# Optimization experiments

Hardware: AMD Instinct MI355X
Metric: run time of the kernel (lower is better)

## Reference

```python
import jax, jax.numpy as jnp
import numpy as np

B, S, D, H = 4, 1024, 1024, 16
HD = D // H  # head_dim = 64


def setup_inputs() -> dict:
    key = jax.random.key(0)
    ks = jax.random.split(key, 12)
    inp = {
        "query": jax.random.normal(ks[0], (B, S, D), jnp.float32),
        "key": jax.random.normal(ks[1], (B, S, D), jnp.float32),
        "value": jax.random.normal(ks[2], (B, S, D), jnp.float32),
        # padding mask: 0 = masked, 1 = keep; broadcastable to [B,H,Sq,Sk]
        "mask": jax.random.randint(ks[3], (B, 1, 1, S), 0, 2, jnp.int32),
        # Dense params (Glorot-ish scale)
        "Wq": jax.random.normal(ks[4], (D, D), jnp.float32) / np.sqrt(D),
        "bq": jnp.zeros((D,), jnp.float32),
        "Wk": jax.random.normal(ks[5], (D, D), jnp.float32) / np.sqrt(D),
        "bk": jnp.zeros((D,), jnp.float32),
        "Wv": jax.random.normal(ks[6], (D, D), jnp.float32) / np.sqrt(D),
        "bv": jnp.zeros((D,), jnp.float32),
        "Wo": jax.random.normal(ks[7], (D, D), jnp.float32) / np.sqrt(D),
        "bo": jnp.zeros((D,), jnp.float32),
    }
    return inp


def _split_heads(x):
    # [B, S, D] -> [B, H, S, HD]
    b, s, _ = x.shape
    return x.reshape(b, s, H, HD).transpose(0, 2, 1, 3)


def reference(query, key, value, mask, Wq, bq, Wk, bk, Wv, bv, Wo, bo):
    q = _split_heads(query @ Wq + bq)   # [B,H,S,HD]
    k = _split_heads(key @ Wk + bk)
    v = _split_heads(value @ Wv + bv)

    scale = jnp.sqrt(jnp.asarray(HD, q.dtype))
    energy = jnp.einsum("bhqd,bhkd->bhqk", q, k) / scale  # [B,H,S,S]
    energy = jnp.where(mask == 0, jnp.asarray(-1e10, energy.dtype), energy)
    attention = jax.nn.softmax(energy, axis=-1)
    # dropout is identity at inference
    x = jnp.einsum("bhqk,bhkd->bhqd", attention, v)       # [B,H,S,HD]
    x = x.transpose(0, 2, 1, 3).reshape(query.shape[0], -1, H * HD)  # [B,S,D]
    outputs = x @ Wo + bo
    return outputs, attention
```

## Files before the change

### kernel.cpp

```cpp
#include <hip/hip_runtime.h>

typedef short short8  __attribute__((ext_vector_type(8)));
typedef short short4v __attribute__((ext_vector_type(4)));
typedef float float4v __attribute__((ext_vector_type(4)));
typedef int   int4v   __attribute__((ext_vector_type(4)));

__device__ __forceinline__ short f2bf(float f) {
    unsigned u = __builtin_bit_cast(unsigned, f);
    u += 0x7fff + ((u >> 16) & 1);
    return (short)(u >> 16);
}

__device__ __forceinline__ void gl_lds16(const void* g, void* l) {
    __builtin_amdgcn_global_load_lds(
        (const __attribute__((address_space(1))) void*)g,
        (__attribute__((address_space(3))) void*)l, 16, 0, 0);
}

__global__ __launch_bounds__(256) void prep(
    const float* __restrict__ W0, const float* __restrict__ W1,
    const float* __restrict__ W2, const float* __restrict__ W3,
    short* __restrict__ T0, short* __restrict__ T1,
    short* __restrict__ T2, short* __restrict__ T3,
    const float* __restrict__ qf, const float* __restrict__ kf,
    const float* __restrict__ vf,
    short* __restrict__ Qb, short* __restrict__ Kb, short* __restrict__ Vb)
{
    __shared__ short Tl[64 * 72];
    const int tid = threadIdx.x;
    if (blockIdx.x >= 1024) {
        int cid = blockIdx.x - 1024;
        int arr = cid >> 11;
        const float* src = arr == 0 ? qf : arr == 1 ? kf : vf;
        short*       dst = arr == 0 ? Qb : arr == 1 ? Kb : Vb;
        size_t base = ((size_t)(cid & 2047) * 256 + tid) * 8;
        float4v v0 = *(const float4v*)&src[base];
        float4v v1 = *(const float4v*)&src[base + 4];
        short8 o = {f2bf(v0[0]), f2bf(v0[1]), f2bf(v0[2]), f2bf(v0[3]),
                    f2bf(v1[0]), f2bf(v1[1]), f2bf(v1[2]), f2bf(v1[3])};
        *(short8*)&dst[base] = o;
        return;
    }
    const int mat = blockIdx.x >> 8;
    const int t   = blockIdx.x & 255;
    const int k0 = (t >> 4) * 64, n0 = (t & 15) * 64;
    const float* W = mat == 0 ? W0 : mat == 1 ? W1 : mat == 2 ? W2 : W3;
    short*       T = mat == 0 ? T0 : mat == 1 ? T1 : mat == 2 ? T2 : T3;
    #pragma unroll
    for (int i = 0; i < 4; i++) {
        int c = tid + i * 256;
        int row = c >> 4, c4 = (c & 15) * 4;
        float4v v = *(const float4v*)&W[(size_t)(k0 + row) * 1024 + n0 + c4];
        short4v s = {f2bf(v[0]), f2bf(v[1]), f2bf(v[2]), f2bf(v[3])};
        *(short4v*)&Tl[row * 72 + c4] = s;
    }
    __syncthreads();
    #pragma unroll
    for (int i = 0; i < 2; i++) {
        int c = tid + i * 256;
        int nrow = c >> 3, k8 = (c & 7) * 8;
        short8 v;
        #pragma unroll
        for (int e = 0; e < 8; e++) v[e] = Tl[(k8 + e) * 72 + nrow];
        *(short8*)&T[(size_t)(n0 + nrow) * 1024 + k0 + k8] = v;
    }
}

__device__ __forceinline__ void gemm_body(
    const short* __restrict__ A, const short* __restrict__ Bt,
    short* As, short* Bs, float4v (&acc)[4][2], int m0, int n0, int K)
{
    const int tid = threadIdx.x;
    const int w = tid >> 6, lid = tid & 63, quad = lid >> 4, l15 = lid & 15;
    const int wr = w >> 1, wc = w & 1;
    const int lrow = lid >> 3, lcb = lid & 7;

    for (int kb = 0; kb < K; kb += 64) {
        #pragma unroll
        for (int p = 0; p < 4; p++) {
            int chunk = p * 4 + w;
            int row = chunk * 8 + lrow;
            int cb = lcb ^ (row & 7);
            gl_lds16(&A[(size_t)(m0 + row) * K + kb + cb * 8], &As[chunk * 512]);
        }
        #pragma unroll
        for (int p = 0; p < 2; p++) {
            int chunk = p * 4 + w;
            int row = chunk * 8 + lrow;
            int cb = lcb ^ (row & 7);
            gl_lds16(&Bt[(size_t)(n0 + row) * K + kb + cb * 8], &Bs[chunk * 512]);
        }
        __syncthreads();

        short8 af[4][2], bfr[2][2];
        #pragma unroll
        for (int i = 0; i < 4; i++) {
            int row = wr * 64 + i * 16 + l15;
            int sw = row & 7;
            #pragma unroll
            for (int h = 0; h < 2; h++)
                af[i][h] = *(short8*)&As[row * 64 + ((h * 4 + quad) ^ sw) * 8];
        }
        #pragma unroll
        for (int j = 0; j < 2; j++) {
            int row = wc * 32 + j * 16 + l15;
            int sw = row & 7;
            #pragma unroll
            for (int h = 0; h < 2; h++)
                bfr[j][h] = *(short8*)&Bs[row * 64 + ((h * 4 + quad) ^ sw) * 8];
        }
        #pragma unroll
        for (int i = 0; i < 4; i++)
            #pragma unroll
            for (int j = 0; j < 2; j++) {
                acc[i][j] = __builtin_amdgcn_mfma_f32_16x16x32_bf16(
                    af[i][0], bfr[j][0], acc[i][j], 0, 0, 0);
                acc[i][j] = __builtin_amdgcn_mfma_f32_16x16x32_bf16(
                    af[i][1], bfr[j][1], acc[i][j], 0, 0, 0);
            }
        __syncthreads();
    }
}

__global__ __launch_bounds__(256) void gemm_qkv(
    const short* __restrict__ Ab, const short* __restrict__ Btb,
    const float* __restrict__ b0, const float* __restrict__ b1,
    const float* __restrict__ b2, short* __restrict__ Cq,
    short* __restrict__ Ck, short* __restrict__ Cvt)
{
    __shared__ short As[128 * 64];
    __shared__ short Bs[64 * 64];
    const int zz = blockIdx.z;
    const short* A  = Ab  + (size_t)zz * 4194304;
    const short* Bt = Btb + (size_t)zz * 1048576;
    const float* bias = zz == 0 ? b0 : zz == 1 ? b1 : b2;
    const int m0 = blockIdx.x * 128, n0 = blockIdx.y * 64;

    float4v acc[4][2];
    #pragma unroll
    for (int i = 0; i < 4; i++)
        #pragma unroll
        for (int j = 0; j < 2; j++) acc[i][j] = (float4v){0.f, 0.f, 0.f, 0.f};

    gemm_body(A, Bt, As, Bs, acc, m0, n0, 1024);

    const int tid = threadIdx.x;
    const int w = tid >> 6, lid = tid & 63, quad = lid >> 4, l15 = lid & 15;
    const int wr = w >> 1, wc = w & 1;
    #pragma unroll
    for (int j = 0; j < 2; j++) {
        int n = n0 + wc * 32 + j * 16 + l15;
        float bj = bias[n];
        #pragma unroll
        for (int i = 0; i < 4; i++) {
            if (zz == 2) {
                int b = m0 >> 10;
                int sbase = (m0 & 1023) + wr * 64 + i * 16 + quad * 4;
                short4v sv;
                #pragma unroll
                for (int r = 0; r < 4; r++) sv[r] = f2bf(acc[i][j][r] + bj);
                *(short4v*)&Cvt[(size_t)b * 1048576 + (size_t)n * 1024 + sbase] = sv;
            } else {
                short* C = zz == 0 ? Cq : Ck;
                #pragma unroll
                for (int r = 0; r < 4; r++) {
                    int m = m0 + wr * 64 + i * 16 + quad * 4 + r;
                    C[(size_t)m * 1024 + n] = f2bf(acc[i][j][r] + bj);
                }
            }
        }
    }
}

__global__ __launch_bounds__(256) void gemm_out(
    const short* __restrict__ A, const short* __restrict__ Bt,
    const float* __restrict__ bias, float* __restrict__ C)
{
    __shared__ short As[128 * 64];
    __shared__ short Bs[64 * 64];
    const int m0 = blockIdx.x * 128, n0 = blockIdx.y * 64;
    float4v acc[4][2];
    #pragma unroll
    for (int i = 0; i < 4; i++)
        #pragma unroll
        for (int j = 0; j < 2; j++) acc[i][j] = (float4v){0.f, 0.f, 0.f, 0.f};

    gemm_body(A, Bt, As, Bs, acc, m0, n0, 1024);

    const int tid = threadIdx.x;
    const int w = tid >> 6, lid = tid & 63, quad = lid >> 4, l15 = lid & 15;
    const int wr = w >> 1, wc = w & 1;
    #pragma unroll
    for (int j = 0; j < 2; j++) {
        int n = n0 + wc * 32 + j * 16 + l15;
        float bj = bias[n];
        #pragma unroll
        for (int i = 0; i < 4; i++)
            #pragma unroll
            for (int r = 0; r < 4; r++) {
                int m = m0 + wr * 64 + i * 16 + quad * 4 + r;
                C[(size_t)m * 1024 + n] = acc[i][j][r] + bj;
            }
    }
}

__global__ __launch_bounds__(256) void attn_kernel(
    const short* __restrict__ Qp, const short* __restrict__ Kp,
    const short* __restrict__ Vt, const int* __restrict__ mask,
    float* __restrict__ attnOut, short* __restrict__ X)
{
    __shared__ float SH[4608];
    __shared__ int   maskl[1024];
    __shared__ float redmx[4][16];
    __shared__ float redsm[4][16];

    const int tid = threadIdx.x;
    const int w = tid >> 6, lid = tid & 63, quad = lid >> 4, l15 = lid & 15;
    const int bid = blockIdx.x;
    const int qb = bid & 63;
    const int bh = bid >> 6;
    const int b = bh >> 4, h = bh & 15;
    const int q0 = qb * 16;
    const size_t rowbase = (size_t)b * 1048576;
    const size_t hoff = (size_t)h * 64;

    *(int4v*)&maskl[tid * 4] = *(const int4v*)&mask[b * 1024 + tid * 4];

    short8 aq0 = *(const short8*)
        &Qp[rowbase + (size_t)(q0 + l15) * 1024 + hoff + quad * 8];
    short8 aq1 = *(const short8*)
        &Qp[rowbase + (size_t)(q0 + l15) * 1024 + hoff + 32 + quad * 8];

    float4v accS[16];
    #pragma unroll
    for (int a = 0; a < 16; a++) accS[a] = (float4v){0.f, 0.f, 0.f, 0.f};

    #pragma unroll
    for (int nk = 0; nk < 8; nk++) {
        #pragma unroll
        for (int jj = 0; jj < 2; jj++) {
            int n = nk * 128 + w * 32 + jj * 16 + l15;
            const short* kr = &Kp[rowbase + (size_t)n * 1024 + hoff + quad * 8];
            short8 b0 = *(const short8*)kr;
            short8 b1 = *(const short8*)(kr + 32);
            int a = nk * 2 + jj;
            accS[a] = __builtin_amdgcn_mfma_f32_16x16x32_bf16(aq0, b0, accS[a], 0, 0, 0);
            accS[a] = __builtin_amdgcn_mfma_f32_16x16x32_bf16(aq1, b1, accS[a], 0, 0, 0);
        }
    }
    __syncthreads();

    float mx[4] = {-3e38f, -3e38f, -3e38f, -3e38f};
    #pragma unroll
    for (int a = 0; a < 16; a++) {
        int col = (a >> 1) * 128 + w * 32 + (a & 1) * 16 + l15;
        bool keep = maskl[col] != 0;
        #pragma unroll
        for (int r = 0; r < 4; r++) {
            float s = accS[a][r] * 0.125f;
            s = keep ? s : -1e10f;
            accS[a][r] = s;
            mx[r] = fmaxf(mx[r], s);
        }
    }
    #pragma unroll
    for (int off = 1; off < 16; off <<= 1)
        #pragma unroll
        for (int r = 0; r < 4; r++) mx[r] = fmaxf(mx[r], __shfl_xor(mx[r], off));
    if (l15 == 0) {
        #pragma unroll
        for (int r = 0; r < 4; r++) redmx[w][quad * 4 + r] = mx[r];
    }
    __syncthreads();
    float mrow[4], sm[4] = {0.f, 0.f, 0.f, 0.f};
    #pragma unroll
    for (int r = 0; r < 4; r++) {
        int qr = quad * 4 + r;
        mrow[r] = fmaxf(fmaxf(redmx[0][qr], redmx[1][qr]),
                        fmaxf(redmx[2][qr], redmx[3][qr]));
    }
    #pragma unroll
    for (int a = 0; a < 16; a++)
        #pragma unroll
        for (int r = 0; r < 4; r++) {
            float e = __expf(accS[a][r] - mrow[r]);
            accS[a][r] = e;
            sm[r] += e;
        }
    #pragma unroll
    for (int off = 1; off < 16; off <<= 1)
        #pragma unroll
        for (int r = 0; r < 4; r++) sm[r] += __shfl_xor(sm[r], off);
    if (l15 == 0) {
        #pragma unroll
        for (int r = 0; r < 4; r++) redsm[w][quad * 4 + r] = sm[r];
    }
    __syncthreads();
    float inv[4];
    #pragma unroll
    for (int r = 0; r < 4; r++) {
        int qr = quad * 4 + r;
        inv[r] = 1.0f / (redsm[0][qr] + redsm[1][qr] + redsm[2][qr] + redsm[3][qr]);
    }

    const size_t abase = ((size_t)bh * 1024 + q0) * 1024;
    float* Pw0 = &SH[(size_t)(0 * 4 + w) * 16 * 36];
    float* Pw1 = &SH[(size_t)(1 * 4 + w) * 16 * 36];
    float4v accA[4], accB[4];
    #pragma unroll
    for (int jj = 0; jj < 4; jj++) {
        accA[jj] = (float4v){0.f, 0.f, 0.f, 0.f};
        accB[jj] = (float4v){0.f, 0.f, 0.f, 0.f};
    }

    #pragma unroll
    for (int t = 0; t < 4; t++) {
        #pragma unroll
        for (int par = 0; par < 2; par++) {
            int kt = t * 2 + par;
            float* Pw = par ? Pw1 : Pw0;
            float4v* accp = par ? accB : accA;
            #pragma unroll
            for (int jj2 = 0; jj2 < 2; jj2++) {
                int a = kt * 2 + jj2;
                #pragma unroll
                for (int r = 0; r < 4; r++)
                    Pw[(quad * 4 + r) * 36 + jj2 * 16 + l15] = accS[a][r] * inv[r];
            }
            #pragma unroll
            for (int pass = 0; pass < 2; pass++) {
                int row = pass * 8 + (lid >> 3), c4 = (lid & 7) * 4;
                float4v pv = *(float4v*)&Pw[row * 36 + c4];
                __builtin_nontemporal_store(pv, (float4v*)
                    &attnOut[abase + (size_t)row * 1024 + kt * 128 + w * 32 + c4]);
            }
            float4v pa0 = *(float4v*)&Pw[l15 * 36 + quad * 8];
            float4v pa1 = *(float4v*)&Pw[l15 * 36 + quad * 8 + 4];
            short8 ap = {f2bf(pa0[0]), f2bf(pa0[1]), f2bf(pa0[2]), f2bf(pa0[3]),
                         f2bf(pa1[0]), f2bf(pa1[1]), f2bf(pa1[2]), f2bf(pa1[3])};
            #pragma unroll
            for (int jj = 0; jj < 4; jj++) {
                short8 bv = *(const short8*)
                    &Vt[rowbase + (hoff + jj * 16 + l15) * 1024 +
                        kt * 128 + w * 32 + quad * 8];
                accp[jj] = __builtin_amdgcn_mfma_f32_16x16x32_bf16(ap, bv, accp[jj], 0, 0, 0);
            }
        }
    }

    __syncthreads();
    float* Xr = SH;
    #pragma unroll
    for (int jj = 0; jj < 4; jj++)
        #pragma unroll
        for (int r = 0; r < 4; r++)
            Xr[(size_t)(w * 16 + quad * 4 + r) * 64 + jj * 16 + l15] =
                accA[jj][r] + accB[jj][r];
    __syncthreads();
    {
        int q = tid >> 4, d4 = (tid & 15) * 4;
        float4v s0 = *(float4v*)&Xr[(size_t)(0 * 16 + q) * 64 + d4];
        float4v s1 = *(float4v*)&Xr[(size_t)(1 * 16 + q) * 64 + d4];
        float4v s2 = *(float4v*)&Xr[(size_t)(2 * 16 + q) * 64 + d4];
        float4v s3 = *(float4v*)&Xr[(size_t)(3 * 16 + q) * 64 + d4];
        short4v o;
        #pragma unroll
        for (int e = 0; e < 4; e++)
            o[e] = f2bf(s0[e] + s1[e] + s2[e] + s3[e]);
        *(short4v*)&X[rowbase + (size_t)(q0 + q) * 1024 + hoff + d4] = o;
    }
}

extern "C" void kernel_launch(void* const* d_in, const int* in_sizes, int n_in,
                              void* d_out, int out_size, void* d_ws, size_t ws_size,
                              hipStream_t stream)
{
    const float* q_in = (const float*)d_in[0];
    const float* k_in = (const float*)d_in[1];
    const float* v_in = (const float*)d_in[2];
    const int*   mask = (const int*)d_in[3];
    const float* Wq = (const float*)d_in[4];
    const float* bq = (const float*)d_in[5];
    const float* Wk = (const float*)d_in[6];
    const float* bk = (const float*)d_in[7];
    const float* Wv = (const float*)d_in[8];
    const float* bv = (const float*)d_in[9];
    const float* Wo = (const float*)d_in[10];
    const float* bo = (const float*)d_in[11];

    short* ws = (short*)d_ws;
    const size_t MEL = 4096ull * 1024;
    short* Qp  = ws;
    short* Kp  = ws + MEL;
    short* Vt  = ws + 2 * MEL;
    short* Xp  = ws + 3 * MEL;
    short* WqT = ws + 4 * MEL;
    short* WkT = WqT + 1024 * 1024;
    short* WvT = WkT + 1024 * 1024;
    short* WoT = WvT + 1024 * 1024;

    float* outp  = (float*)d_out;
    float* attnp = outp + MEL;

    short* Qb = (short*)attnp;
    short* Kb = Qb + MEL;
    short* Vb = Kb + MEL;

    prep<<<dim3(7168), dim3(256), 0, stream>>>(Wq, Wk, Wv, Wo,
                                               WqT, WkT, WvT, WoT,
                                               q_in, k_in, v_in, Qb, Kb, Vb);
    gemm_qkv<<<dim3(32, 16, 3), 256, 0, stream>>>(Qb, WqT, bq, bk, bv,
                                                  Qp, Kp, Vt);
    attn_kernel<<<dim3(4096), dim3(256), 0, stream>>>(Qp, Kp, Vt, mask, attnp, Xp);
    gemm_out<<<dim3(32, 16), 256, 0, stream>>>(Xp, WoT, bo, outp);
}
```

Before: 499.9 us.

## Recompute QK^T in a two-pass online softmax to cut register pressure

The attention kernel no longer keeps all 16 score tiles in registers. A first pass computes QK^T with an online running max and sum, then the block reduces those statistics. A second pass recomputes QK^T to produce normalized probabilities, store them and feed the PV MFMAs. Launch bounds now request 4 blocks per CU, and the split accumulators are merged into one. This trades doubled QK MFMA work and K reloads, plus extra exp calls, for lower VGPR use and higher occupancy.

Result: slower. 547.6 us (+9.5%).

```diff
diff --git a/kernel.cpp b/kernel.cpp
--- a/kernel.cpp
+++ b/kernel.cpp
@@ -204,15 +204,15 @@
     }
 }
 
-__global__ __launch_bounds__(256) void attn_kernel(
+__global__ __launch_bounds__(256, 4) void attn_kernel(
     const short* __restrict__ Qp, const short* __restrict__ Kp,
     const short* __restrict__ Vt, const int* __restrict__ mask,
     float* __restrict__ attnOut, short* __restrict__ X)
 {
     __shared__ float SH[4608];
     __shared__ int   maskl[1024];
-    __shared__ float redmx[4][16];
-    __shared__ float redsm[4][16];
+    __shared__ float redm[4][16];
+    __shared__ float redl[4][16];
 
     const int tid = threadIdx.x;
     const int w = tid >> 6, lid = tid & 63, quad = lid >> 4, l15 = lid & 15;
@@ -230,121 +230,107 @@
         &Qp[rowbase + (size_t)(q0 + l15) * 1024 + hoff + quad * 8];
     short8 aq1 = *(const short8*)
         &Qp[rowbase + (size_t)(q0 + l15) * 1024 + hoff + 32 + quad * 8];
-
-    float4v accS[16];
-    #pragma unroll
-    for (int a = 0; a < 16; a++) accS[a] = (float4v){0.f, 0.f, 0.f, 0.f};
-
+    __syncthreads();
+
+    float m_r[4] = {-3e38f, -3e38f, -3e38f, -3e38f};
+    float l_r[4] = {0.f, 0.f, 0.f, 0.f};
     #pragma unroll
     for (int nk = 0; nk < 8; nk++) {
         #pragma unroll
         for (int jj = 0; jj < 2; jj++) {
             int n = nk * 128 + w * 32 + jj * 16 + l15;
             const short* kr = &Kp[rowbase + (size_t)n * 1024 + hoff + quad * 8];
-            short8 b0 = *(const short8*)kr;
-            short8 b1 = *(const short8*)(kr + 32);
-            int a = nk * 2 + jj;
-            accS[a] = __builtin_amdgcn_mfma_f32_16x16x32_bf16(aq0, b0, accS[a], 0, 0, 0);
-            accS[a] = __builtin_amdgcn_mfma_f32_16x16x32_bf16(aq1, b1, accS[a], 0, 0, 0);
+            short8 kf0 = *(const short8*)kr;
+            short8 kf1 = *(const short8*)(kr + 32);
+            float4v acc = (float4v){0.f, 0.f, 0.f, 0.f};
+            acc = __builtin_amdgcn_mfma_f32_16x16x32_bf16(aq0, kf0, acc, 0, 0, 0);
+            acc = __builtin_amdgcn_mfma_f32_16x16x32_bf16(aq1, kf1, acc, 0, 0, 0);
+            bool keep = maskl[n] != 0;
+            #pragma unroll
+            for (int r = 0; r < 4; r++) {
+                float s = keep ? acc[r] * 0.125f : -1e10f;
+                float mn = fmaxf(m_r[r], s);
+                l_r[r] = l_r[r] * __expf(m_r[r] - mn) + __expf(s - mn);
+                m_r[r] = mn;
+            }
+        }
+    }
+    #pragma unroll
+    for (int off = 1; off < 16; off <<= 1) {
+        #pragma unroll
+        for (int r = 0; r < 4; r++) {
+            float mo = __shfl_xor(m_r[r], off);
+            float lo = __shfl_xor(l_r[r], off);
+            float mn = fmaxf(m_r[r], mo);
+            l_r[r] = l_r[r] * __expf(m_r[r] - mn) + lo * __expf(mo - mn);
+            m_r[r] = mn;
+        }
+    }
+    if (l15 == 0) {
+        #pragma unroll
+        for (int r = 0; r < 4; r++) {
+            redm[w][quad * 4 + r] = m_r[r];
+            redl[w][quad * 4 + r] = l_r[r];
         }
     }
     __syncthreads();
-
-    float mx[4] = {-3e38f, -3e38f, -3e38f, -3e38f};
-    #pragma unroll
-    for (int a = 0; a < 16; a++) {
-        int col = (a >> 1) * 128 + w * 32 + (a & 1) * 16 + l15;
-        bool keep = maskl[col] != 0;
-        #pragma unroll
-        for (int r = 0; r < 4; r++) {
-            float s = accS[a][r] * 0.125f;
-            s = keep ? s : -1e10f;
-            accS[a][r] = s;
-            mx[r] = fmaxf(mx[r], s);
-        }
-    }
-    #pragma unroll
-    for (int off = 1; off < 16; off <<= 1)
-        #pragma unroll
-        for (int r = 0; r < 4; r++) mx[r] = fmaxf(mx[r], __shfl_xor(mx[r], off));
-    if (l15 == 0) {
-        #pragma unroll
-        for (int r = 0; r < 4; r++) redmx[w][quad * 4 + r] = mx[r];
-    }
-    __syncthreads();
-    float mrow[4], sm[4] = {0.f, 0.f, 0.f, 0.f};
+    float mrow[4], inv[4];
     #pragma unroll
     for (int r = 0; r < 4; r++) {
         int qr = quad * 4 + r;
-        mrow[r] = fmaxf(fmaxf(redmx[0][qr], redmx[1][qr]),
-                        fmaxf(redmx[2][qr], redmx[3][qr]));
-    }
-    #pragma unroll
-    for (int a = 0; a < 16; a++)
-        #pragma unroll
-        for (int r = 0; r < 4; r++) {
-            float e = __expf(accS[a][r] - mrow[r]);
-            accS[a][r] = e;
-            sm[r] += e;
-        }
-    #pragma unroll
-    for (int off = 1; off < 16; off <<= 1)
-        #pragma unroll
-        for (int r = 0; r < 4; r++) sm[r] += __shfl_xor(sm[r], off);
-    if (l15 == 0) {
-        #pragma unroll
-        for (int r = 0; r < 4; r++) redsm[w][quad * 4 + r] = sm[r];
-    }
-    __syncthreads();
-    float inv[4];
-    #pragma unroll
-    for (int r = 0; r < 4; r++) {
-        int qr = quad * 4 + r;
-        inv[r] = 1.0f / (redsm[0][qr] + redsm[1][qr] + redsm[2][qr] + redsm[3][qr]);
+        float m0 = redm[0][qr], m1 = redm[1][qr];
+        float m2 = redm[2][qr], m3 = redm[3][qr];
+        float M = fmaxf(fmaxf(m0, m1), fmaxf(m2, m3));
+        float L = redl[0][qr] * __expf(m0 - M) + redl[1][qr] * __expf(m1 - M)
+                + redl[2][qr] * __expf(m2 - M) + redl[3][qr] * __expf(m3 - M);
+        mrow[r] = M;
+        inv[r] = 1.0f / L;
     }
 
     const size_t abase = ((size_t)bh * 1024 + q0) * 1024;
     float* Pw0 = &SH[(size_t)(0 * 4 + w) * 16 * 36];
     float* Pw1 = &SH[(size_t)(1 * 4 + w) * 16 * 36];
-    float4v accA[4], accB[4];
-    #pragma unroll
-    for (int jj = 0; jj < 4; jj++) {
-        accA[jj] = (float4v){0.f, 0.f, 0.f, 0.f};
-        accB[jj] = (float4v){0.f, 0.f, 0.f, 0.f};
-    }
-
-    #pragma unroll
-    for (int t = 0; t < 4; t++) {
-        #pragma unroll
-        for (int par = 0; par < 2; par++) {
-            int kt = t * 2 + par;
-            float* Pw = par ? Pw1 : Pw0;
-            float4v* accp = par ? accB : accA;
-            #pragma unroll
-            for (int jj2 = 0; jj2 < 2; jj2++) {
-                int a = kt * 2 + jj2;
-                #pragma unroll
-                for (int r = 0; r < 4; r++)
-                    Pw[(quad * 4 + r) * 36 + jj2 * 16 + l15] = accS[a][r] * inv[r];
+    float4v accX[4];
+    #pragma unroll
+    for (int jj = 0; jj < 4; jj++) accX[jj] = (float4v){0.f, 0.f, 0.f, 0.f};
+
+    #pragma unroll
+    for (int kt = 0; kt < 8; kt++) {
+        float* Pw = (kt & 1) ? Pw1 : Pw0;
+        #pragma unroll
+        for (int jj2 = 0; jj2 < 2; jj2++) {
+            int n = kt * 128 + w * 32 + jj2 * 16 + l15;
+            const short* kr = &Kp[rowbase + (size_t)n * 1024 + hoff + quad * 8];
+            short8 kf0 = *(const short8*)kr;
+            short8 kf1 = *(const short8*)(kr + 32);
+            float4v acc = (float4v){0.f, 0.f, 0.f, 0.f};
+            acc = __builtin_amdgcn_mfma_f32_16x16x32_bf16(aq0, kf0, acc, 0, 0, 0);
+            acc = __builtin_amdgcn_mfma_f32_16x16x32_bf16(aq1, kf1, acc, 0, 0, 0);
+            bool keep = maskl[n] != 0;
+            #pragma unroll
+            for (int r = 0; r < 4; r++) {
+                float s = keep ? acc[r] * 0.125f : -1e10f;
+                float p = __expf(s - mrow[r]) * inv[r];
+                Pw[(quad * 4 + r) * 36 + jj2 * 16 + l15] = p;
             }
-            #pragma unroll
-            for (int pass = 0; pass < 2; pass++) {
-                int row = pass * 8 + (lid >> 3), c4 = (lid & 7) * 4;
-                float4v pv = *(float4v*)&Pw[row * 36 + c4];
-                __builtin_nontemporal_store(pv, (float4v*)
-                    &attnOut[abase + (size_t)row * 1024 + kt * 128 + w * 32 + c4]);
-            }
-            float4v pa0 = *(float4v*)&Pw[l15 * 36 + quad * 8];
-            float4v pa1 = *(float4v*)&Pw[l15 * 36 + quad * 8 + 4];
-            short8 ap = {f2bf(pa0[0]), f2bf(pa0[1]), f2bf(pa0[2]), f2bf(pa0[3]),
-                         f2bf(pa1[0]), f2bf(pa1[1]), f2bf(pa1[2]), f2bf(pa1[3])};
-            #pragma unroll
-            for (int jj = 0; jj < 4; jj++) {
-                short8 bv = *(const short8*)
-                    &Vt[rowbase + (hoff + jj * 16 + l15) * 1024 +
-                        kt * 128 + w * 32 + quad * 8];
-                accp[jj] = __builtin_amdgcn_mfma_f32_16x16x32_bf16(ap, bv, accp[jj], 0, 0, 0);
-            }
+        }
+        #pragma unroll
+        for (int pass = 0; pass < 2; pass++) {
+            int row = pass * 8 + (lid >> 3), c4 = (lid & 7) * 4;
+            float4v pv = *(float4v*)&Pw[row * 36 + c4];
+            __builtin_nontemporal_store(pv, (float4v*)
+                &attnOut[abase + (size_t)row * 1024 + kt * 128 + w * 32 + c4]);
+        }
+        float4v pa0 = *(float4v*)&Pw[l15 * 36 + quad * 8];
+        float4v pa1 = *(float4v*)&Pw[l15 * 36 + quad * 8 + 4];
+        short8 ap = {f2bf(pa0[0]), f2bf(pa0[1]), f2bf(pa0[2]), f2bf(pa0[3]),
+                     f2bf(pa1[0]), f2bf(pa1[1]), f2bf(pa1[2]), f2bf(pa1[3])};
+        #pragma unroll
+        for (int jj = 0; jj < 4; jj++) {
+            short8 bv = *(const short8*)
+                &Vt[rowbase + (hoff + jj * 16 + l15) * 1024 +
+                    kt * 128 + w * 32 + quad * 8];
+            accX[jj] = __builtin_amdgcn_mfma_f32_16x16x32_bf16(ap, bv, accX[jj], 0, 0, 0);
         }
     }
 
@@ -354,8 +340,7 @@
     for (int jj = 0; jj < 4; jj++)
         #pragma unroll
         for (int r = 0; r < 4; r++)
-            Xr[(size_t)(w * 16 + quad * 4 + r) * 64 + jj * 16 + l15] =
-                accA[jj][r] + accB[jj][r];
+            Xr[(size_t)(w * 16 + quad * 4 + r) * 64 + jj * 16 + l15] = accX[jj][r];
     __syncthreads();
     {
         int q = tid >> 4, d4 = (tid & 15) * 4;
```
